# Performance work log

Hardware: AMD Instinct MI355X
Metric: run time of the kernel (lower is better)

Reference implementation:

```python
import jax, jax.numpy as jnp
import numpy as np

B, S_ENC, S_DEC, D_ENC, D_DEC, UNITS = 8, 256, 128, 512, 512, 512


def setup_inputs() -> dict:
    key = jax.random.key(0)
    ks = jax.random.split(key, 5)
    enc_scale = 1.0 / np.sqrt(D_ENC)
    dec_scale = 1.0 / np.sqrt(D_DEC)
    u_scale = 1.0 / np.sqrt(UNITS)
    return {
        "encodings": jax.random.normal(ks[0], (B, S_ENC, D_ENC), dtype=jnp.float32),
        "decodings": jax.random.normal(ks[1], (B, S_DEC, D_DEC), dtype=jnp.float32),
        "W_enc": jax.random.normal(ks[2], (D_ENC, UNITS), dtype=jnp.float32) * enc_scale,
        "W_dec": jax.random.normal(ks[3], (D_DEC, UNITS), dtype=jnp.float32) * dec_scale,
        "W_score": jax.random.normal(ks[4], (UNITS, 1), dtype=jnp.float32) * u_scale,
        "bias_enc": jnp.zeros((UNITS,), dtype=jnp.float32),
        "bias_dec": jnp.zeros((UNITS,), dtype=jnp.float32),
        "bias_score": jnp.zeros((1,), dtype=jnp.float32),
    }


def reference(encodings, decodings, W_enc, W_dec, W_score, bias_enc, bias_dec, bias_score):
    # activation='linear' -> identity after the bias add
    d_enc = jnp.einsum("bed,du->beu", encodings, W_enc) + bias_enc  # [B, S_enc, U]
    d_dec = jnp.einsum("bqd,du->bqu", decodings, W_dec) + bias_dec  # [B, S_dec, U]
    # Bahdanau additive scores: tanh(dec_proj + enc_proj) broadcast to [B, S_dec, S_enc, U]
    tanh_add = jnp.tanh(d_dec[:, :, None, :] + d_enc[:, None, :, :])
    scores = jnp.einsum("bqeu,u->bqe", tanh_add, W_score[:, 0]) + bias_score[0]
    weights = jax.nn.softmax(scores, axis=-1)  # softmax over encoder positions
    # weighted sum of raw encodings -> [B, S_dec, D_enc]
    contexts = jnp.einsum("bqe,bed->bqd", weights, encodings)
    return contexts
```

## Files before the change

kernel.cpp:

```cpp
#include <hip/hip_runtime.h>
#include <hip/hip_fp16.h>

typedef __attribute__((ext_vector_type(8))) _Float16 f16x8;
typedef __attribute__((ext_vector_type(4))) float f32x4;
typedef __attribute__((ext_vector_type(2))) __fp16 fp16x2;

__device__ inline unsigned int pack_f16(float x, float y) {
    union { fp16x2 h; unsigned int u; } c;
    c.h = __builtin_amdgcn_cvt_pkrtz(x, y);
    return c.u;
}
__device__ inline float2 unpack_f16(unsigned int u) {
    union { unsigned int u32; __half2 h2; } c; c.u32 = u;
    return __half22float2(c.h2);
}

__global__ __launch_bounds__(256) void prep_w(
    const float* __restrict__ Wenc, const float* __restrict__ Wdec,
    const float* __restrict__ enc,  const float* __restrict__ dec,
    unsigned short* __restrict__ WeT, unsigned short* __restrict__ WdT,
    unsigned short* __restrict__ enc16, unsigned short* __restrict__ dec16)
{
    __shared__ float L[64][65];
    const int bid = blockIdx.x;
    const int t = threadIdx.x;
    if (bid >= 128) {
        const float* src; unsigned int* dst;
        if (bid < 192) { int blk = bid - 128; src = enc + (size_t)blk * 16384;
                         dst = (unsigned int*)enc16 + (size_t)blk * 8192; }
        else           { int blk = bid - 192; src = dec + (size_t)blk * 16384;
                         dst = (unsigned int*)dec16 + (size_t)blk * 8192; }
#pragma unroll 4
        for (int i = 0; i < 16; ++i) {
            int off = (i << 10) + (t << 2);
            float4 v = *(const float4*)(src + off);
            *(uint2*)(dst + (off >> 1)) =
                make_uint2(pack_f16(v.x, v.y), pack_f16(v.z, v.w));
        }
        return;
    }
    const float* W = (bid < 64) ? Wenc : Wdec;
    unsigned short* T = (bid < 64) ? WeT : WdT;
    const int tb = bid & 63;
    const int d0 = (tb >> 3) << 6, u0v = (tb & 7) << 6;
    {
        const int c4 = (t & 15) << 2;
#pragma unroll
        for (int i = 0; i < 4; ++i) {
            int row = (i << 4) + (t >> 4);
            float4 v = *(const float4*)&W[(size_t)(d0 + row) * 512 + u0v + c4];
            L[row][c4 + 0] = v.x;
            L[row][c4 + 1] = v.y;
            L[row][c4 + 2] = v.z;
            L[row][c4 + 3] = v.w;
        }
    }
    __syncthreads();
    const int u = t >> 2, dg = t & 3;
    unsigned int hw[8];
#pragma unroll
    for (int j = 0; j < 8; ++j) {
        float x0 = L[(dg << 4) + (j << 1) + 0][u];
        float x1 = L[(dg << 4) + (j << 1) + 1][u];
        hw[j] = pack_f16(x0, x1);
    }
    size_t ob = (size_t)(u0v + u) * 512 + d0 + (dg << 4);
    *(uint4*)&T[ob]     = make_uint4(hw[0], hw[1], hw[2], hw[3]);
    *(uint4*)&T[ob + 8] = make_uint4(hw[4], hw[5], hw[6], hw[7]);
}

__global__ __launch_bounds__(128, 1) void proj_kernel(
    const unsigned short* __restrict__ enc16, const unsigned short* __restrict__ dec16,
    const unsigned short* __restrict__ WeT,   const unsigned short* __restrict__ WdT,
    const float* __restrict__ bias_enc, const float* __restrict__ bias_dec,
    unsigned short* __restrict__ EH,
    float* __restrict__ Gq4)
{
    const float Cs = 2.8853900817779268f;
    const int bid = blockIdx.x;
    const int t = threadIdx.x;
    const int lane = t & 63, wr = t >> 6;
    const int frow = lane & 15, quad = lane >> 4;
    const int ko = quad << 3;

    const unsigned short *pa0, *pa1, *pb0, *pb1;
    if (bid < 512) {
        const int b = bid & 7, s = bid >> 3;
        const int u0 = ((s & 7) << 6) + (wr << 5);
        const int e0 = (s >> 3) << 5;
        pa0 = WeT + (size_t)(u0 + frow) * 512 + ko;
        pa1 = pa0 + 16 * 512;
        pb0 = enc16 + (size_t)((b << 8) + e0 + frow) * 512 + ko;
        pb1 = pb0 + 16 * 512;
    } else {
        const int s = bid - 512;
        const int b = s & 7, s2 = s >> 3;
        const int q0 = ((s2 >> 4) << 6) + (wr << 5);
        const int u0 = (s2 & 15) << 5;
        pa0 = dec16 + (size_t)((b << 7) + q0 + frow) * 512 + ko;
        pa1 = pa0 + 16 * 512;
        pb0 = WdT + (size_t)(u0 + frow) * 512 + ko;
        pb1 = pb0 + 16 * 512;
    }

    f16x8 sa0[4], sa1[4], sb0[4], sb1[4];
    auto LD = [&](int st, int k) {
        sa0[st] = *(const f16x8*)(pa0 + k);
        sa1[st] = *(const f16x8*)(pa1 + k);
        sb0[st] = *(const f16x8*)(pb0 + k);
        sb1[st] = *(const f16x8*)(pb1 + k);
    };
    f32x4 acc[2][2] = {{{0.f,0.f,0.f,0.f},{0.f,0.f,0.f,0.f}},
                       {{0.f,0.f,0.f,0.f},{0.f,0.f,0.f,0.f}}};
    LD(0, 0); LD(1, 32); LD(2, 64); LD(3, 96);
    for (int k0 = 0; k0 < 512; k0 += 128) {
#pragma unroll
        for (int st = 0; st < 4; ++st) {
            acc[0][0] = __builtin_amdgcn_mfma_f32_16x16x32_f16(sa0[st], sb0[st], acc[0][0], 0, 0, 0);
            acc[0][1] = __builtin_amdgcn_mfma_f32_16x16x32_f16(sa0[st], sb1[st], acc[0][1], 0, 0, 0);
            acc[1][0] = __builtin_amdgcn_mfma_f32_16x16x32_f16(sa1[st], sb0[st], acc[1][0], 0, 0, 0);
            acc[1][1] = __builtin_amdgcn_mfma_f32_16x16x32_f16(sa1[st], sb1[st], acc[1][1], 0, 0, 0);
            LD(st, (k0 + 128 + (st << 5)) & 511);
        }
    }

    if (bid < 512) {
        const int b = bid & 7, s = bid >> 3;
        const int u0 = ((s & 7) << 6) + (wr << 5);
        const int e0 = (s >> 3) << 5;
#pragma unroll
        for (int fm = 0; fm < 2; ++fm)
#pragma unroll
            for (int fn = 0; fn < 2; ++fn) {
                int ub = u0 + (fm << 4) + (quad << 2);
                int e  = e0 + (fn << 4) + frow;
                float4 bi = *(const float4*)&bias_enc[ub];
                float E0 = __builtin_amdgcn_exp2f((acc[fm][fn][0] + bi.x) * Cs);
                float E1 = __builtin_amdgcn_exp2f((acc[fm][fn][1] + bi.y) * Cs);
                float E2 = __builtin_amdgcn_exp2f((acc[fm][fn][2] + bi.z) * Cs);
                float E3 = __builtin_amdgcn_exp2f((acc[fm][fn][3] + bi.w) * Cs);
                ((uint2*)EH)[(((size_t)(b << 7) + (ub >> 2)) << 8) + e] =
                    make_uint2(pack_f16(E0, E1), pack_f16(E2, E3));
            }
    } else {
        const int s = bid - 512;
        const int b = s & 7, s2 = s >> 3;
        const int q0 = ((s2 >> 4) << 6) + (wr << 5);
        const int u0 = (s2 & 15) << 5;
#pragma unroll
        for (int fm = 0; fm < 2; ++fm)
#pragma unroll
            for (int fn = 0; fn < 2; ++fn) {
                int qb = q0 + (fm << 4) + (quad << 2);
                int u  = u0 + (fn << 4) + frow;
                float bi = bias_dec[u];
                size_t base = (((size_t)(b << 5) + (qb >> 2)) << 11) + (u << 2);
#pragma unroll
                for (int g = 0; g < 4; ++g)
                    Gq4[base + g] =
                        __builtin_amdgcn_exp2f((acc[fm][fn][g] + bi) * Cs);
            }
    }
}

__global__ __launch_bounds__(1024, 4) void attend_kernel(
    const unsigned short* __restrict__ enc16,
    const unsigned short* __restrict__ EH,
    const float* __restrict__ Gq4,
    const float* __restrict__ Wscore,
    float* __restrict__ out)
{
    __shared__ float smem[8192];
    __shared__ float wT[256][4];

    const float LOG2E = 1.4426950408889634f;

    const int bid = blockIdx.x;
    const int b = bid & 7;
    const int qt = (bid >> 3) & 31;
    const int q0 = qt << 2;
    const int tid = threadIdx.x;
    const int wv = tid >> 6, lane = tid & 63;

    const int e  = ((wv & 3) << 6) + lane;
    const int uq = wv >> 2;
    const int u0 = __builtin_amdgcn_readfirstlane(uq << 7);

    const uint2* Ep = (const uint2*)EH + (((size_t)(b << 7) + (u0 >> 2)) << 8) + e;
    const float* Gq = Gq4 + (((size_t)(b << 5) + qt) << 11);
    const float* Wp = Wscore + u0;

    float a0 = 0.f, a1 = 0.f, a2 = 0.f, a3 = 0.f;
    uint2 de = Ep[0];
    float4 g0 = *(const float4*)(Gq + ((u0 + 0) << 2));
    float4 g1 = *(const float4*)(Gq + ((u0 + 1) << 2));
    float4 g2 = *(const float4*)(Gq + ((u0 + 2) << 2));
    float4 g3 = *(const float4*)(Gq + ((u0 + 3) << 2));
    float4 w4 = *(const float4*)(Wp);
    for (int g = 0; g < 32; ++g) {
        uint2 cde = de;
        float4 cg0 = g0, cg1 = g1, cg2 = g2, cg3 = g3, cw = w4;
        if (g < 31) {
            int un = u0 + ((g + 1) << 2);
            de = Ep[(size_t)(g + 1) << 8];
            g0 = *(const float4*)(Gq + ((un + 0) << 2));
            g1 = *(const float4*)(Gq + ((un + 1) << 2));
            g2 = *(const float4*)(Gq + ((un + 2) << 2));
            g3 = *(const float4*)(Gq + ((un + 3) << 2));
            w4 = *(const float4*)(Wp + (g + 1 - g/32) * 0 + ((g + 1) << 2));
        }
        float2 f01 = unpack_f16(cde.x);
        float2 f23 = unpack_f16(cde.y);
        float E;
        E = f01.x;
        a0 = fmaf(cw.x, __builtin_amdgcn_rcpf(fmaf(E, cg0.x, 1.f)), a0);
        a1 = fmaf(cw.x, __builtin_amdgcn_rcpf(fmaf(E, cg0.y, 1.f)), a1);
        a2 = fmaf(cw.x, __builtin_amdgcn_rcpf(fmaf(E, cg0.z, 1.f)), a2);
        a3 = fmaf(cw.x, __builtin_amdgcn_rcpf(fmaf(E, cg0.w, 1.f)), a3);
        E = f01.y;
        a0 = fmaf(cw.y, __builtin_amdgcn_rcpf(fmaf(E, cg1.x, 1.f)), a0);
        a1 = fmaf(cw.y, __builtin_amdgcn_rcpf(fmaf(E, cg1.y, 1.f)), a1);
        a2 = fmaf(cw.y, __builtin_amdgcn_rcpf(fmaf(E, cg1.z, 1.f)), a2);
        a3 = fmaf(cw.y, __builtin_amdgcn_rcpf(fmaf(E, cg1.w, 1.f)), a3);
        E = f23.x;
        a0 = fmaf(cw.z, __builtin_amdgcn_rcpf(fmaf(E, cg2.x, 1.f)), a0);
        a1 = fmaf(cw.z, __builtin_amdgcn_rcpf(fmaf(E, cg2.y, 1.f)), a1);
        a2 = fmaf(cw.z, __builtin_amdgcn_rcpf(fmaf(E, cg2.z, 1.f)), a2);
        a3 = fmaf(cw.z, __builtin_amdgcn_rcpf(fmaf(E, cg2.w, 1.f)), a3);
        E = f23.y;
        a0 = fmaf(cw.w, __builtin_amdgcn_rcpf(fmaf(E, cg3.x, 1.f)), a0);
        a1 = fmaf(cw.w, __builtin_amdgcn_rcpf(fmaf(E, cg3.y, 1.f)), a1);
        a2 = fmaf(cw.w, __builtin_amdgcn_rcpf(fmaf(E, cg3.z, 1.f)), a2);
        a3 = fmaf(cw.w, __builtin_amdgcn_rcpf(fmaf(E, cg3.w, 1.f)), a3);
    }
    smem[((uq << 2) + 0) * 256 + e] = a0;
    smem[((uq << 2) + 1) * 256 + e] = a1;
    smem[((uq << 2) + 2) * 256 + e] = a2;
    smem[((uq << 2) + 3) * 256 + e] = a3;
    __syncthreads();

    if (wv < 4) {
        const int q = wv;
        float l[4];
        float m = -1e30f;
#pragma unroll
        for (int i = 0; i < 4; ++i) {
            int ee = lane + (i << 6);
            float a = smem[(0 + q) * 256 + ee] + smem[(4 + q) * 256 + ee] +
                      smem[(8 + q) * 256 + ee] + smem[(12 + q) * 256 + ee];
            l[i] = -2.f * a;
            m = fmaxf(m, l[i]);
        }
#pragma unroll
        for (int mk = 32; mk >= 1; mk >>= 1) m = fmaxf(m, __shfl_xor(m, mk, 64));
        float p[4];
        float ssum = 0.f;
#pragma unroll
        for (int i = 0; i < 4; ++i) {
            p[i] = __builtin_amdgcn_exp2f((l[i] - m) * LOG2E);
            ssum += p[i];
        }
#pragma unroll
        for (int mk = 32; mk >= 1; mk >>= 1) ssum += __shfl_xor(ssum, mk, 64);
        float inv = __builtin_amdgcn_rcpf(ssum);
#pragma unroll
        for (int i = 0; i < 4; ++i) wT[lane + (i << 6)][q] = p[i] * inv;
    }
    __syncthreads();

    {
        const int dp = tid & 255;
        float p0x = 0.f, p0y = 0.f, p1x = 0.f, p1y = 0.f;
        float p2x = 0.f, p2y = 0.f, p3x = 0.f, p3y = 0.f;
        const unsigned int* ep = (const unsigned int*)enc16 +
                                 (((size_t)(b << 8) + (uq << 6)) << 8) + dp;
#pragma unroll 4
        for (int ee = 0; ee < 64; ++ee) {
            float2 x = unpack_f16(ep[(size_t)ee << 8]);
            float4 w = *(const float4*)&wT[(uq << 6) + ee][0];
            p0x = fmaf(w.x, x.x, p0x); p0y = fmaf(w.x, x.y, p0y);
            p1x = fmaf(w.y, x.x, p1x); p1y = fmaf(w.y, x.y, p1y);
            p2x = fmaf(w.z, x.x, p2x); p2y = fmaf(w.z, x.y, p2y);
            p3x = fmaf(w.w, x.x, p3x); p3y = fmaf(w.w, x.y, p3y);
        }
        float2* sc = (float2*)smem;
        sc[((uq << 2) + 0) * 256 + dp] = make_float2(p0x, p0y);
        sc[((uq << 2) + 1) * 256 + dp] = make_float2(p1x, p1y);
        sc[((uq << 2) + 2) * 256 + dp] = make_float2(p2x, p2y);
        sc[((uq << 2) + 3) * 256 + dp] = make_float2(p3x, p3y);
        __syncthreads();
        const int q = tid >> 8;
        float2 s0 = sc[(0 + q) * 256 + dp];
        float2 s1 = sc[(4 + q) * 256 + dp];
        float2 s2 = sc[(8 + q) * 256 + dp];
        float2 s3 = sc[(12 + q) * 256 + dp];
        float2 o = make_float2(s0.x + s1.x + s2.x + s3.x,
                               s0.y + s1.y + s2.y + s3.y);
        *(float2*)&out[(size_t)((b << 7) + q0 + q) * 512 + (dp << 1)] = o;
    }
}

extern "C" void kernel_launch(void* const* d_in, const int* in_sizes, int n_in,
                              void* d_out, int out_size, void* d_ws, size_t ws_size,
                              hipStream_t stream) {
    const float* enc      = (const float*)d_in[0];
    const float* dec      = (const float*)d_in[1];
    const float* Wenc     = (const float*)d_in[2];
    const float* Wdec     = (const float*)d_in[3];
    const float* Wscore   = (const float*)d_in[4];
    const float* bias_enc = (const float*)d_in[5];
    const float* bias_dec = (const float*)d_in[6];
    float* out = (float*)d_out;

    float* ws = (float*)d_ws;
    unsigned short* EH  = (unsigned short*)ws;
    float* Gq4          = ws + 524288;
    unsigned short* WeT = (unsigned short*)(ws + 1048576);
    unsigned short* WdT = WeT + 262144;
    unsigned short* enc16 = WdT + 262144;
    unsigned short* dec16 = enc16 + 1048576;

    prep_w<<<224, 256, 0, stream>>>(Wenc, Wdec, enc, dec, WeT, WdT, enc16, dec16);
    proj_kernel<<<768, 128, 0, stream>>>(enc16, dec16, WeT, WdT,
                                         bias_enc, bias_dec, EH, Gq4);
    attend_kernel<<<256, 1024, 0, stream>>>(enc16, EH, Gq4, Wscore, out);
}
```

Baseline: 110.0 us.

## Shrink projection tiles to one MFMA per wave and double-buffer attend loads

The projection kernel switches from 2x2 MFMA tiles per wave in 128-thread blocks to a single 16x16 tile per wave in 256-thread blocks with 6-block occupancy and twice the grid. This is meant to raise parallelism and latency hiding, at the cost of reusing each loaded fragment less. The decoder-side output now uses a vectorized float4 store. The attend loop is unrolled by two with two encoder-value buffers in flight, so loads are prefetched further ahead of the arithmetic.

```diff
diff --git a/kernel.cpp b/kernel.cpp
--- a/kernel.cpp
+++ b/kernel.cpp
@@ -69,7 +69,7 @@
     *(uint4*)&T[ob + 8] = make_uint4(hw[4], hw[5], hw[6], hw[7]);
 }
 
-__global__ __launch_bounds__(128, 1) void proj_kernel(
+__global__ __launch_bounds__(256, 6) void proj_kernel(
     const unsigned short* __restrict__ enc16, const unsigned short* __restrict__ dec16,
     const unsigned short* __restrict__ WeT,   const unsigned short* __restrict__ WdT,
     const float* __restrict__ bias_enc, const float* __restrict__ bias_dec,
@@ -79,87 +79,67 @@
     const float Cs = 2.8853900817779268f;
     const int bid = blockIdx.x;
     const int t = threadIdx.x;
-    const int lane = t & 63, wr = t >> 6;
+    const int lane = t & 63, wv = t >> 6;
     const int frow = lane & 15, quad = lane >> 4;
     const int ko = quad << 3;
 
-    const unsigned short *pa0, *pa1, *pb0, *pb1;
-    if (bid < 512) {
-        const int b = bid & 7, s = bid >> 3;
-        const int u0 = ((s & 7) << 6) + (wr << 5);
-        const int e0 = (s >> 3) << 5;
-        pa0 = WeT + (size_t)(u0 + frow) * 512 + ko;
-        pa1 = pa0 + 16 * 512;
-        pb0 = enc16 + (size_t)((b << 8) + e0 + frow) * 512 + ko;
-        pb1 = pb0 + 16 * 512;
+    const bool is_enc = (bid < 1024);
+    int u0, e0, q0, b;
+    const unsigned short *pa, *pb;
+    if (is_enc) {
+        b = bid & 7;
+        const int s = bid >> 3;
+        const int ut = s >> 2;
+        const int et = ((s & 3) << 2) + wv;
+        u0 = ut << 4; e0 = et << 4; q0 = 0;
+        pa = WeT + (size_t)(u0 + frow) * 512 + ko;
+        pb = enc16 + (size_t)((b << 8) + e0 + frow) * 512 + ko;
     } else {
-        const int s = bid - 512;
-        const int b = s & 7, s2 = s >> 3;
-        const int q0 = ((s2 >> 4) << 6) + (wr << 5);
-        const int u0 = (s2 & 15) << 5;
-        pa0 = dec16 + (size_t)((b << 7) + q0 + frow) * 512 + ko;
-        pa1 = pa0 + 16 * 512;
-        pb0 = WdT + (size_t)(u0 + frow) * 512 + ko;
-        pb1 = pb0 + 16 * 512;
-    }
-
-    f16x8 sa0[4], sa1[4], sb0[4], sb1[4];
+        const int bid2 = bid - 1024;
+        b = bid2 & 7;
+        const int s = bid2 >> 3;
+        const int qt = s >> 3;
+        const int ut = ((s & 7) << 2) + wv;
+        q0 = qt << 4; u0 = ut << 4; e0 = 0;
+        pa = dec16 + (size_t)((b << 7) + q0 + frow) * 512 + ko;
+        pb = WdT + (size_t)(u0 + frow) * 512 + ko;
+    }
+
+    f16x8 sa[4], sb[4];
     auto LD = [&](int st, int k) {
-        sa0[st] = *(const f16x8*)(pa0 + k);
-        sa1[st] = *(const f16x8*)(pa1 + k);
-        sb0[st] = *(const f16x8*)(pb0 + k);
-        sb1[st] = *(const f16x8*)(pb1 + k);
+        sa[st] = *(const f16x8*)(pa + k);
+        sb[st] = *(const f16x8*)(pb + k);
     };
-    f32x4 acc[2][2] = {{{0.f,0.f,0.f,0.f},{0.f,0.f,0.f,0.f}},
-                       {{0.f,0.f,0.f,0.f},{0.f,0.f,0.f,0.f}}};
+    f32x4 acc = {0.f, 0.f, 0.f, 0.f};
     LD(0, 0); LD(1, 32); LD(2, 64); LD(3, 96);
     for (int k0 = 0; k0 < 512; k0 += 128) {
 #pragma unroll
         for (int st = 0; st < 4; ++st) {
-            acc[0][0] = __builtin_amdgcn_mfma_f32_16x16x32_f16(sa0[st], sb0[st], acc[0][0], 0, 0, 0);
-            acc[0][1] = __builtin_amdgcn_mfma_f32_16x16x32_f16(sa0[st], sb1[st], acc[0][1], 0, 0, 0);
-            acc[1][0] = __builtin_amdgcn_mfma_f32_16x16x32_f16(sa1[st], sb0[st], acc[1][0], 0, 0, 0);
-            acc[1][1] = __builtin_amdgcn_mfma_f32_16x16x32_f16(sa1[st], sb1[st], acc[1][1], 0, 0, 0);
+            acc = __builtin_amdgcn_mfma_f32_16x16x32_f16(sa[st], sb[st], acc, 0, 0, 0);
             LD(st, (k0 + 128 + (st << 5)) & 511);
         }
     }
 
-    if (bid < 512) {
-        const int b = bid & 7, s = bid >> 3;
-        const int u0 = ((s & 7) << 6) + (wr << 5);
-        const int e0 = (s >> 3) << 5;
-#pragma unroll
-        for (int fm = 0; fm < 2; ++fm)
-#pragma unroll
-            for (int fn = 0; fn < 2; ++fn) {
-                int ub = u0 + (fm << 4) + (quad << 2);
-                int e  = e0 + (fn << 4) + frow;
-                float4 bi = *(const float4*)&bias_enc[ub];
-                float E0 = __builtin_amdgcn_exp2f((acc[fm][fn][0] + bi.x) * Cs);
-                float E1 = __builtin_amdgcn_exp2f((acc[fm][fn][1] + bi.y) * Cs);
-                float E2 = __builtin_amdgcn_exp2f((acc[fm][fn][2] + bi.z) * Cs);
-                float E3 = __builtin_amdgcn_exp2f((acc[fm][fn][3] + bi.w) * Cs);
-                ((uint2*)EH)[(((size_t)(b << 7) + (ub >> 2)) << 8) + e] =
-                    make_uint2(pack_f16(E0, E1), pack_f16(E2, E3));
-            }
+    if (is_enc) {
+        const int ub = u0 + (quad << 2);
+        const int e  = e0 + frow;
+        float4 bi = *(const float4*)&bias_enc[ub];
+        float E0 = __builtin_amdgcn_exp2f((acc[0] + bi.x) * Cs);
+        float E1 = __builtin_amdgcn_exp2f((acc[1] + bi.y) * Cs);
+        float E2 = __builtin_amdgcn_exp2f((acc[2] + bi.z) * Cs);
+        float E3 = __builtin_amdgcn_exp2f((acc[3] + bi.w) * Cs);
+        ((uint2*)EH)[(((size_t)(b << 7) + (ub >> 2)) << 8) + e] =
+            make_uint2(pack_f16(E0, E1), pack_f16(E2, E3));
     } else {
-        const int s = bid - 512;
-        const int b = s & 7, s2 = s >> 3;
-        const int q0 = ((s2 >> 4) << 6) + (wr << 5);
-        const int u0 = (s2 & 15) << 5;
-#pragma unroll
-        for (int fm = 0; fm < 2; ++fm)
-#pragma unroll
-            for (int fn = 0; fn < 2; ++fn) {
-                int qb = q0 + (fm << 4) + (quad << 2);
-                int u  = u0 + (fn << 4) + frow;
-                float bi = bias_dec[u];
-                size_t base = (((size_t)(b << 5) + (qb >> 2)) << 11) + (u << 2);
-#pragma unroll
-                for (int g = 0; g < 4; ++g)
-                    Gq4[base + g] =
-                        __builtin_amdgcn_exp2f((acc[fm][fn][g] + bi) * Cs);
-            }
+        const int qb = q0 + (quad << 2);
+        const int u  = u0 + frow;
+        float bi = bias_dec[u];
+        float G0 = __builtin_amdgcn_exp2f((acc[0] + bi) * Cs);
+        float G1 = __builtin_amdgcn_exp2f((acc[1] + bi) * Cs);
+        float G2 = __builtin_amdgcn_exp2f((acc[2] + bi) * Cs);
+        float G3 = __builtin_amdgcn_exp2f((acc[3] + bi) * Cs);
+        size_t base = (((size_t)(b << 5) + (qb >> 2)) << 11) + ((size_t)u << 2);
+        *(float4*)&Gq4[base] = make_float4(G0, G1, G2, G3);
     }
 }
 
@@ -191,24 +171,16 @@
     const float* Wp = Wscore + u0;
 
     float a0 = 0.f, a1 = 0.f, a2 = 0.f, a3 = 0.f;
-    uint2 de = Ep[0];
+    uint2 deA = Ep[0];
+    uint2 deB = Ep[1 << 8];
     float4 g0 = *(const float4*)(Gq + ((u0 + 0) << 2));
     float4 g1 = *(const float4*)(Gq + ((u0 + 1) << 2));
     float4 g2 = *(const float4*)(Gq + ((u0 + 2) << 2));
     float4 g3 = *(const float4*)(Gq + ((u0 + 3) << 2));
     float4 w4 = *(const float4*)(Wp);
-    for (int g = 0; g < 32; ++g) {
-        uint2 cde = de;
-        float4 cg0 = g0, cg1 = g1, cg2 = g2, cg3 = g3, cw = w4;
-        if (g < 31) {
-            int un = u0 + ((g + 1) << 2);
-            de = Ep[(size_t)(g + 1) << 8];
-            g0 = *(const float4*)(Gq + ((un + 0) << 2));
-            g1 = *(const float4*)(Gq + ((un + 1) << 2));
-            g2 = *(const float4*)(Gq + ((un + 2) << 2));
-            g3 = *(const float4*)(Gq + ((un + 3) << 2));
-            w4 = *(const float4*)(Wp + (g + 1 - g/32) * 0 + ((g + 1) << 2));
-        }
+
+    auto PROC = [&](uint2 cde, float4 cg0, float4 cg1, float4 cg2, float4 cg3,
+                    float4 cw) {
         float2 f01 = unpack_f16(cde.x);
         float2 f23 = unpack_f16(cde.y);
         float E;
@@ -232,6 +204,34 @@
         a1 = fmaf(cw.w, __builtin_amdgcn_rcpf(fmaf(E, cg3.y, 1.f)), a1);
         a2 = fmaf(cw.w, __builtin_amdgcn_rcpf(fmaf(E, cg3.z, 1.f)), a2);
         a3 = fmaf(cw.w, __builtin_amdgcn_rcpf(fmaf(E, cg3.w, 1.f)), a3);
+    };
+
+    for (int g = 0; g < 32; g += 2) {
+        uint2 cde = deA;
+        float4 cg0 = g0, cg1 = g1, cg2 = g2, cg3 = g3, cw = w4;
+        deA = Ep[(size_t)((g + 2) & 31) << 8];
+        {
+            int un = u0 + ((g + 1) << 2);
+            g0 = *(const float4*)(Gq + ((un + 0) << 2));
+            g1 = *(const float4*)(Gq + ((un + 1) << 2));
+            g2 = *(const float4*)(Gq + ((un + 2) << 2));
+            g3 = *(const float4*)(Gq + ((un + 3) << 2));
+            w4 = *(const float4*)(Wp + ((g + 1) << 2));
+        }
+        PROC(cde, cg0, cg1, cg2, cg3, cw);
+
+        cde = deB;
+        cg0 = g0; cg1 = g1; cg2 = g2; cg3 = g3; cw = w4;
+        deB = Ep[(size_t)((g + 3) & 31) << 8];
+        if (g < 30) {
+            int un = u0 + ((g + 2) << 2);
+            g0 = *(const float4*)(Gq + ((un + 0) << 2));
+            g1 = *(const float4*)(Gq + ((un + 1) << 2));
+            g2 = *(const float4*)(Gq + ((un + 2) << 2));
+            g3 = *(const float4*)(Gq + ((un + 3) << 2));
+            w4 = *(const float4*)(Wp + ((g + 2) << 2));
+        }
+        PROC(cde, cg0, cg1, cg2, cg3, cw);
     }
     smem[((uq << 2) + 0) * 256 + e] = a0;
     smem[((uq << 2) + 1) * 256 + e] = a1;
@@ -321,7 +321,7 @@
     unsigned short* dec16 = enc16 + 1048576;
 
     prep_w<<<224, 256, 0, stream>>>(Wenc, Wdec, enc, dec, WeT, WdT, enc16, dec16);
-    proj_kernel<<<768, 128, 0, stream>>>(enc16, dec16, WeT, WdT,
-                                         bias_enc, bias_dec, EH, Gq4);
+    proj_kernel<<<1536, 256, 0, stream>>>(enc16, dec16, WeT, WdT,
+                                          bias_enc, bias_dec, EH, Gq4);
     attend_kernel<<<256, 1024, 0, stream>>>(enc16, EH, Gq4, Wscore, out);
 }
```

New measurement: 121.3 us. 10.2% more time.

## Split proj GEMM K across wave pairs, vectorize Gq4 stores, double-buffer attend loads

Applied to the files above, without the earlier changes.

The projection kernel now launches 256 threads per block, and two wave pairs each handle half of the K dimension. Partial accumulators are reduced through shared memory, which doubles the waves available to hide latency on the short K=512 GEMM. Gq4 outputs are written as float4 instead of scalar stores. The attend loop is unrolled by two with separate prefetch registers for the EH loads, which adds prefetch depth. The cost is an extra LDS round-trip and barrier in the projection kernel, plus higher register use in attend.

```diff
diff --git a/kernel.cpp b/kernel.cpp
--- a/kernel.cpp
+++ b/kernel.cpp
@@ -69,37 +69,42 @@
     *(uint4*)&T[ob + 8] = make_uint4(hw[4], hw[5], hw[6], hw[7]);
 }
 
-__global__ __launch_bounds__(128, 1) void proj_kernel(
+__global__ __launch_bounds__(256, 3) void proj_kernel(
     const unsigned short* __restrict__ enc16, const unsigned short* __restrict__ dec16,
     const unsigned short* __restrict__ WeT,   const unsigned short* __restrict__ WdT,
     const float* __restrict__ bias_enc, const float* __restrict__ bias_dec,
     unsigned short* __restrict__ EH,
     float* __restrict__ Gq4)
 {
+    __shared__ float red[2][64][17];
+
     const float Cs = 2.8853900817779268f;
     const int bid = blockIdx.x;
     const int t = threadIdx.x;
-    const int lane = t & 63, wr = t >> 6;
+    const int lane = t & 63, wv = t >> 6;
+    const int th = wv & 1;
+    const int kh = wv >> 1;
+    const int koff = kh << 8;
     const int frow = lane & 15, quad = lane >> 4;
     const int ko = quad << 3;
 
     const unsigned short *pa0, *pa1, *pb0, *pb1;
     if (bid < 512) {
         const int b = bid & 7, s = bid >> 3;
-        const int u0 = ((s & 7) << 6) + (wr << 5);
+        const int u0 = ((s & 7) << 6) + (th << 5);
         const int e0 = (s >> 3) << 5;
-        pa0 = WeT + (size_t)(u0 + frow) * 512 + ko;
+        pa0 = WeT + (size_t)(u0 + frow) * 512 + ko + koff;
         pa1 = pa0 + 16 * 512;
-        pb0 = enc16 + (size_t)((b << 8) + e0 + frow) * 512 + ko;
+        pb0 = enc16 + (size_t)((b << 8) + e0 + frow) * 512 + ko + koff;
         pb1 = pb0 + 16 * 512;
     } else {
         const int s = bid - 512;
         const int b = s & 7, s2 = s >> 3;
-        const int q0 = ((s2 >> 4) << 6) + (wr << 5);
+        const int q0 = ((s2 >> 4) << 6) + (th << 5);
         const int u0 = (s2 & 15) << 5;
-        pa0 = dec16 + (size_t)((b << 7) + q0 + frow) * 512 + ko;
+        pa0 = dec16 + (size_t)((b << 7) + q0 + frow) * 512 + ko + koff;
         pa1 = pa0 + 16 * 512;
-        pb0 = WdT + (size_t)(u0 + frow) * 512 + ko;
+        pb0 = WdT + (size_t)(u0 + frow) * 512 + ko + koff;
         pb1 = pb0 + 16 * 512;
     }
 
@@ -113,20 +118,39 @@
     f32x4 acc[2][2] = {{{0.f,0.f,0.f,0.f},{0.f,0.f,0.f,0.f}},
                        {{0.f,0.f,0.f,0.f},{0.f,0.f,0.f,0.f}}};
     LD(0, 0); LD(1, 32); LD(2, 64); LD(3, 96);
-    for (int k0 = 0; k0 < 512; k0 += 128) {
+    for (int k0 = 0; k0 < 256; k0 += 128) {
 #pragma unroll
         for (int st = 0; st < 4; ++st) {
             acc[0][0] = __builtin_amdgcn_mfma_f32_16x16x32_f16(sa0[st], sb0[st], acc[0][0], 0, 0, 0);
             acc[0][1] = __builtin_amdgcn_mfma_f32_16x16x32_f16(sa0[st], sb1[st], acc[0][1], 0, 0, 0);
             acc[1][0] = __builtin_amdgcn_mfma_f32_16x16x32_f16(sa1[st], sb0[st], acc[1][0], 0, 0, 0);
             acc[1][1] = __builtin_amdgcn_mfma_f32_16x16x32_f16(sa1[st], sb1[st], acc[1][1], 0, 0, 0);
-            LD(st, (k0 + 128 + (st << 5)) & 511);
-        }
-    }
+            LD(st, (k0 + 128 + (st << 5)) & 255);
+        }
+    }
+
+    if (kh == 1) {
+#pragma unroll
+        for (int fm = 0; fm < 2; ++fm)
+#pragma unroll
+            for (int fn = 0; fn < 2; ++fn)
+#pragma unroll
+                for (int g = 0; g < 4; ++g)
+                    red[th][lane][(((fm << 1) + fn) << 2) + g] = acc[fm][fn][g];
+    }
+    __syncthreads();
+    if (kh == 1) return;
+#pragma unroll
+    for (int fm = 0; fm < 2; ++fm)
+#pragma unroll
+        for (int fn = 0; fn < 2; ++fn)
+#pragma unroll
+            for (int g = 0; g < 4; ++g)
+                acc[fm][fn][g] += red[th][lane][(((fm << 1) + fn) << 2) + g];
 
     if (bid < 512) {
         const int b = bid & 7, s = bid >> 3;
-        const int u0 = ((s & 7) << 6) + (wr << 5);
+        const int u0 = ((s & 7) << 6) + (th << 5);
         const int e0 = (s >> 3) << 5;
 #pragma unroll
         for (int fm = 0; fm < 2; ++fm)
@@ -145,7 +169,7 @@
     } else {
         const int s = bid - 512;
         const int b = s & 7, s2 = s >> 3;
-        const int q0 = ((s2 >> 4) << 6) + (wr << 5);
+        const int q0 = ((s2 >> 4) << 6) + (th << 5);
         const int u0 = (s2 & 15) << 5;
 #pragma unroll
         for (int fm = 0; fm < 2; ++fm)
@@ -154,11 +178,12 @@
                 int qb = q0 + (fm << 4) + (quad << 2);
                 int u  = u0 + (fn << 4) + frow;
                 float bi = bias_dec[u];
-                size_t base = (((size_t)(b << 5) + (qb >> 2)) << 11) + (u << 2);
-#pragma unroll
-                for (int g = 0; g < 4; ++g)
-                    Gq4[base + g] =
-                        __builtin_amdgcn_exp2f((acc[fm][fn][g] + bi) * Cs);
+                float G0 = __builtin_amdgcn_exp2f((acc[fm][fn][0] + bi) * Cs);
+                float G1 = __builtin_amdgcn_exp2f((acc[fm][fn][1] + bi) * Cs);
+                float G2 = __builtin_amdgcn_exp2f((acc[fm][fn][2] + bi) * Cs);
+                float G3 = __builtin_amdgcn_exp2f((acc[fm][fn][3] + bi) * Cs);
+                size_t base = (((size_t)(b << 5) + (qb >> 2)) << 11) + ((size_t)u << 2);
+                *(float4*)&Gq4[base] = make_float4(G0, G1, G2, G3);
             }
     }
 }
@@ -191,24 +216,16 @@
     const float* Wp = Wscore + u0;
 
     float a0 = 0.f, a1 = 0.f, a2 = 0.f, a3 = 0.f;
-    uint2 de = Ep[0];
+    uint2 deA = Ep[0];
+    uint2 deB = Ep[1 << 8];
     float4 g0 = *(const float4*)(Gq + ((u0 + 0) << 2));
     float4 g1 = *(const float4*)(Gq + ((u0 + 1) << 2));
     float4 g2 = *(const float4*)(Gq + ((u0 + 2) << 2));
     float4 g3 = *(const float4*)(Gq + ((u0 + 3) << 2));
     float4 w4 = *(const float4*)(Wp);
-    for (int g = 0; g < 32; ++g) {
-        uint2 cde = de;
-        float4 cg0 = g0, cg1 = g1, cg2 = g2, cg3 = g3, cw = w4;
-        if (g < 31) {
-            int un = u0 + ((g + 1) << 2);
-            de = Ep[(size_t)(g + 1) << 8];
-            g0 = *(const float4*)(Gq + ((un + 0) << 2));
-            g1 = *(const float4*)(Gq + ((un + 1) << 2));
-            g2 = *(const float4*)(Gq + ((un + 2) << 2));
-            g3 = *(const float4*)(Gq + ((un + 3) << 2));
-            w4 = *(const float4*)(Wp + (g + 1 - g/32) * 0 + ((g + 1) << 2));
-        }
+
+    auto PROC = [&](uint2 cde, float4 cg0, float4 cg1, float4 cg2, float4 cg3,
+                    float4 cw) {
         float2 f01 = unpack_f16(cde.x);
         float2 f23 = unpack_f16(cde.y);
         float E;
@@ -232,6 +249,34 @@
         a1 = fmaf(cw.w, __builtin_amdgcn_rcpf(fmaf(E, cg3.y, 1.f)), a1);
         a2 = fmaf(cw.w, __builtin_amdgcn_rcpf(fmaf(E, cg3.z, 1.f)), a2);
         a3 = fmaf(cw.w, __builtin_amdgcn_rcpf(fmaf(E, cg3.w, 1.f)), a3);
+    };
+
+    for (int g = 0; g < 32; g += 2) {
+        uint2 cde = deA;
+        float4 cg0 = g0, cg1 = g1, cg2 = g2, cg3 = g3, cw = w4;
+        deA = Ep[(size_t)((g + 2) & 31) << 8];
+        {
+            int un = u0 + ((g + 1) << 2);
+            g0 = *(const float4*)(Gq + ((un + 0) << 2));
+            g1 = *(const float4*)(Gq + ((un + 1) << 2));
+            g2 = *(const float4*)(Gq + ((un + 2) << 2));
+            g3 = *(const float4*)(Gq + ((un + 3) << 2));
+            w4 = *(const float4*)(Wp + ((g + 1) << 2));
+        }
+        PROC(cde, cg0, cg1, cg2, cg3, cw);
+
+        cde = deB;
+        cg0 = g0; cg1 = g1; cg2 = g2; cg3 = g3; cw = w4;
+        deB = Ep[(size_t)((g + 3) & 31) << 8];
+        if (g < 30) {
+            int un = u0 + ((g + 2) << 2);
+            g0 = *(const float4*)(Gq + ((un + 0) << 2));
+            g1 = *(const float4*)(Gq + ((un + 1) << 2));
+            g2 = *(const float4*)(Gq + ((un + 2) << 2));
+            g3 = *(const float4*)(Gq + ((un + 3) << 2));
+            w4 = *(const float4*)(Wp + ((g + 2) << 2));
+        }
+        PROC(cde, cg0, cg1, cg2, cg3, cw);
     }
     smem[((uq << 2) + 0) * 256 + e] = a0;
     smem[((uq << 2) + 1) * 256 + e] = a1;
@@ -321,7 +366,7 @@
     unsigned short* dec16 = enc16 + 1048576;
 
     prep_w<<<224, 256, 0, stream>>>(Wenc, Wdec, enc, dec, WeT, WdT, enc16, dec16);
-    proj_kernel<<<768, 128, 0, stream>>>(enc16, dec16, WeT, WdT,
+    proj_kernel<<<768, 256, 0, stream>>>(enc16, dec16, WeT, WdT,
                                          bias_enc, bias_dec, EH, Gq4);
     attend_kernel<<<256, 1024, 0, stream>>>(enc16, EH, Gq4, Wscore, out);
 }
```

New measurement: 111.7 us. No clear change (+1.5%).
